# Kernel optimization log

Hardware: AMD Instinct MI355X
Metric: run time of the kernel (lower is better)

Reference implementation:

```python
import jax, jax.numpy as jnp
import numpy as np

HEADS, KV_HEADS, HEAD_DIM = 16, 4, 128
WINDOW, ROPE_THETA, EPS = 512, 10000.0, 1e-6


def _rms_norm(x, w):
    # Gemma RMSNorm: float32 compute, scale = 1 + w
    xf = x.astype(jnp.float32)
    y = xf * jax.lax.rsqrt(jnp.mean(xf * xf, axis=-1, keepdims=True) + EPS)
    return (y * (1.0 + w.astype(jnp.float32))).astype(x.dtype)


def _rope_cos_sin(T, dtype):
    inv_freq = 1.0 / ROPE_THETA ** (jnp.arange(0, HEAD_DIM, 2, dtype=jnp.float32) / HEAD_DIM)
    pos = jnp.arange(T, dtype=jnp.float32)
    freqs = pos[:, None] * inv_freq[None, :]          # [T, Dh/2]
    emb = jnp.concatenate([freqs, freqs], axis=-1)    # [T, Dh]
    return emb.astype(dtype), emb  # cos/sin applied below


def _rotate_half(x):
    x1, x2 = jnp.split(x, 2, axis=-1)
    return jnp.concatenate([-x2, x1], axis=-1)


def setup_inputs() -> dict:
    key = jax.random.key(0)
    ks = jax.random.split(key, 7)
    B, T, D = 2, 2048, 2048
    s = lambda k, shape, fan: jax.random.normal(k, shape, jnp.float32) * (fan ** -0.5)
    return {
        "x": jax.random.normal(ks[0], (B, T, D), jnp.float32),
        "Wq": s(ks[1], (HEADS * HEAD_DIM, D), D),
        "Wk": s(ks[2], (KV_HEADS * HEAD_DIM, D), D),
        "Wv": s(ks[3], (KV_HEADS * HEAD_DIM, D), D),
        "Wo": s(ks[4], (D, HEADS * HEAD_DIM), HEADS * HEAD_DIM),
        "qn_w": jax.random.normal(ks[5], (HEAD_DIM,), jnp.float32) * 0.02,
        "kn_w": jax.random.normal(ks[6], (HEAD_DIM,), jnp.float32) * 0.02,
    }


def reference(x, Wq, Wk, Wv, Wo, qn_w, kn_w):
    B, T, D = x.shape
    H, Hkv, Dh = HEADS, KV_HEADS, HEAD_DIM
    G = H // Hkv

    q = (x @ Wq.T).reshape(B, T, H, Dh).transpose(0, 2, 1, 3)     # [B,H,T,Dh]
    k = (x @ Wk.T).reshape(B, T, Hkv, Dh).transpose(0, 2, 1, 3)   # [B,Hkv,T,Dh]
    v = (x @ Wv.T).reshape(B, T, Hkv, Dh).transpose(0, 2, 1, 3)

    q = _rms_norm(q, qn_w)
    k = _rms_norm(k, kn_w)

    emb_c, emb_f = _rope_cos_sin(T, x.dtype)
    cos = jnp.cos(emb_f).astype(x.dtype)[None, None]  # [1,1,T,Dh]
    sin = jnp.sin(emb_f).astype(x.dtype)[None, None]
    q = q * cos + _rotate_half(q) * sin
    k = k * cos + _rotate_half(k) * sin

    q = q * (Dh ** -0.5)
    qg = q.reshape(B, Hkv, G, T, Dh)

    scores = jnp.einsum('bhgtd,bhkd->bhgtk', qg.astype(jnp.float32), k.astype(jnp.float32))

    dist = jnp.arange(T)[:, None] - jnp.arange(T)[None, :]        # [T,T]
    mask = (dist >= 0) & (dist <= WINDOW)
    scores = jnp.where(mask[None, None, None], scores, jnp.finfo(jnp.float32).min)
    att = jax.nn.softmax(scores, axis=-1).astype(x.dtype)

    ctx = jnp.einsum('bhgtk,bhkd->bhgtd', att, v)                 # [B,Hkv,G,T,Dh]
    out = ctx.reshape(B, H, T, Dh).transpose(0, 2, 1, 3).reshape(B, T, H * Dh)
    return out @ Wo.T
```

## Files before the change

### kernel.cpp

```cpp
#include <hip/hip_runtime.h>
#include <stdint.h>


typedef __attribute__((ext_vector_type(8))) short bf16x8;
typedef __attribute__((ext_vector_type(4))) float f32x4;

typedef __attribute__((address_space(3))) unsigned int lds_u32;
typedef const __attribute__((address_space(1))) unsigned int glb_u32;

#define LOG2E 1.44269504088896340736f

__device__ __forceinline__ unsigned short f2bf(float f) {
  unsigned int x = __builtin_bit_cast(unsigned int, f);
  x += 0x7FFFu + ((x >> 16) & 1u);
  return (unsigned short)(x >> 16);
}

__global__ __launch_bounds__(256) void castall(const float* __restrict__ x,
                                               const float* __restrict__ wq,
                                               const float* __restrict__ wk,
                                               const float* __restrict__ wv,
                                               const float* __restrict__ wo,
                                               unsigned short* __restrict__ xb,
                                               unsigned short* __restrict__ wqkvb,
                                               unsigned short* __restrict__ wob) {
  int i = blockIdx.x * 256 + threadIdx.x;
  const float* src;
  unsigned short* dst;
  int off;
  if (i < 2097152)       { src = x;  dst = xb;              off = i; }
  else if (i < 3145728)  { src = wq; dst = wqkvb;           off = i - 2097152; }
  else if (i < 3407872)  { src = wk; dst = wqkvb + 4194304; off = i - 3145728; }
  else if (i < 3670016)  { src = wv; dst = wqkvb + 5242880; off = i - 3407872; }
  else                   { src = wo; dst = wob;             off = i - 3670016; }
  float4 v = ((const float4*)src)[off];
  uint2 o;
  o.x = (unsigned)f2bf(v.x) | ((unsigned)f2bf(v.y) << 16);
  o.y = (unsigned)f2bf(v.z) | ((unsigned)f2bf(v.w) << 16);
  ((uint2*)dst)[off] = o;
}

__global__ __launch_bounds__(256) void rope_tab(float* __restrict__ c,
                                                float* __restrict__ s) {
  int idx = blockIdx.x * 256 + threadIdx.x;
  int t = idx >> 6, i = idx & 63;
  float invf = exp2f(-(float)i * (13.287712379549449f / 64.0f));
  float a = (float)t * invf;
  c[idx] = cosf(a);
  s[idx] = sinf(a);
}

template <int BN>
__global__ __launch_bounds__(512, 2) void gemm256(const unsigned short* __restrict__ A,
                                                  const unsigned short* __restrict__ Bm,
                                                  float* __restrict__ C,
                                                  int N, int K) {
  constexpr int BSL = BN * 128;
  __shared__ uint8_t lds[65536 + 2 * BSL];
  const int tid = threadIdx.x, lane = tid & 63, w = tid >> 6;
  const int wm = w >> 2, wn = w & 3;
  const size_t m0 = (size_t)blockIdx.y * 256, n0 = (size_t)blockIdx.x * BN;
  const int srow = lane >> 3;
  const int schunk = (lane & 7) ^ srow;

  f32x4 acc[8][BN / 64];
#pragma unroll
  for (int i = 0; i < 8; ++i)
#pragma unroll
    for (int j = 0; j < BN / 64; ++j) acc[i][j] = f32x4{0.f, 0.f, 0.f, 0.f};

  const int NT = K >> 6;

  auto stageA = [&](int t, int par) {
    uint8_t* slot = lds + (par << 15);
#pragma unroll
    for (int j = 0; j < 4; ++j) {
      int r0 = (j * 8 + w) * 8;
      const unsigned short* src =
          A + (m0 + r0 + srow) * (size_t)K + t * 64 + schunk * 8;
      __builtin_amdgcn_global_load_lds((glb_u32*)src,
                                       (lds_u32*)(slot + r0 * 128), 16, 0, 0);
    }
  };
  auto stageB = [&](int t, int par) {
    uint8_t* slot = lds + 65536 + par * BSL;
#pragma unroll
    for (int j = 0; j < BN / 64; ++j) {
      int r0 = (j * 8 + w) * 8;
      const unsigned short* src =
          Bm + (n0 + r0 + srow) * (size_t)K + t * 64 + schunk * 8;
      __builtin_amdgcn_global_load_lds((glb_u32*)src,
                                       (lds_u32*)(slot + r0 * 128), 16, 0, 0);
    }
  };
  auto compute = [&](int par, int h) {
    const uint8_t* Asl = lds + (par << 15);
    const uint8_t* Bsl = lds + 65536 + par * BSL;
    bf16x8 af[8], bf[BN / 64];
    const int x7 = lane & 7;
    const int cx = h * 4 + (lane >> 4);
    const int rab = wm * 128 + (lane & 15);
    const int rbb = wn * (BN / 4) + (lane & 15);
#pragma unroll
    for (int mt = 0; mt < 8; ++mt)
      af[mt] = *(const bf16x8*)(Asl + (rab + mt * 16) * 128 + ((cx ^ x7) << 4));
#pragma unroll
    for (int nt = 0; nt < BN / 64; ++nt)
      bf[nt] = *(const bf16x8*)(Bsl + (rbb + nt * 16) * 128 + ((cx ^ x7) << 4));
    __builtin_amdgcn_s_setprio(1);
#pragma unroll
    for (int mt = 0; mt < 8; ++mt)
#pragma unroll
      for (int nt = 0; nt < BN / 64; ++nt)
        acc[mt][nt] = __builtin_amdgcn_mfma_f32_16x16x32_bf16(
            af[mt], bf[nt], acc[mt][nt], 0, 0, 0);
    __builtin_amdgcn_s_setprio(0);
  };

  stageA(0, 0);
  stageB(0, 0);
  for (int t = 0; t < NT - 1; ++t) {
    const int p = t & 1, q = p ^ 1;
    stageA(t + 1, q);
    asm volatile("s_waitcnt vmcnt(4)" ::: "memory");
    __builtin_amdgcn_s_barrier();
    __builtin_amdgcn_sched_barrier(0);
    compute(p, 0);
    stageB(t + 1, q);
    compute(p, 1);
    asm volatile("" ::: "memory");
    __builtin_amdgcn_s_barrier();
    __builtin_amdgcn_sched_barrier(0);
  }
  {
    const int p = (NT - 1) & 1;
    asm volatile("s_waitcnt vmcnt(0)" ::: "memory");
    __builtin_amdgcn_s_barrier();
    __builtin_amdgcn_sched_barrier(0);
    compute(p, 0);
    compute(p, 1);
  }
#pragma unroll
  for (int mt = 0; mt < 8; ++mt)
#pragma unroll
    for (int nt = 0; nt < BN / 64; ++nt) {
      size_t row = m0 + wm * 128 + mt * 16 + (lane >> 4) * 4;
      size_t col = n0 + wn * (BN / 4) + nt * 16 + (lane & 15);
#pragma unroll
      for (int r = 0; r < 4; ++r)
        C[(row + r) * N + col] = acc[mt][nt][r];
    }
}

__global__ __launch_bounds__(256) void eplg(const float* __restrict__ qkv,
                                            const float* __restrict__ qw,
                                            const float* __restrict__ kw,
                                            const float* __restrict__ rc,
                                            const float* __restrict__ rs,
                                            unsigned short* __restrict__ qb,
                                            unsigned short* __restrict__ kb) {
  const int row = blockIdx.x;
  const int t = row & 2047;
  const int lane = threadIdx.x & 63, w = threadIdx.x >> 6;
  const float* base = qkv + (size_t)row * 3072;
  const int d0 = 2 * lane;
  const float c0 = rc[t * 64 + (d0 & 63)];
  const float c1 = rc[t * 64 + ((d0 + 1) & 63)];
  const float s0 = rs[t * 64 + (d0 & 63)];
  const float s1 = rs[t * 64 + ((d0 + 1) & 63)];
  const float sgn = (lane < 32) ? -1.0f : 1.0f;

#pragma unroll
  for (int hh = 0; hh < 4; ++hh) {
    int h = w * 4 + hh;
    float2 x = *(const float2*)(base + h * 128 + d0);
    float ss = x.x * x.x + x.y * x.y;
#pragma unroll
    for (int m = 1; m < 64; m <<= 1) ss += __shfl_xor(ss, m);
    float r = rsqrtf(ss * (1.0f / 128.0f) + 1e-6f);
    float y0 = x.x * r * (1.0f + qw[d0]);
    float y1 = x.y * r * (1.0f + qw[d0 + 1]);
    float p0 = __shfl_xor(y0, 32);
    float p1 = __shfl_xor(y1, 32);
    float o0 = (y0 * c0 + sgn * p0 * s0) * 0.08838834764831845f;
    float o1 = (y1 * c1 + sgn * p1 * s1) * 0.08838834764831845f;
    unsigned int pk = (unsigned)f2bf(o0) | ((unsigned)f2bf(o1) << 16);
    *(unsigned int*)(qb + (size_t)row * 2048 + h * 128 + d0) = pk;
  }
  {
    float2 x = *(const float2*)(base + 2048 + w * 128 + d0);
    float ss = x.x * x.x + x.y * x.y;
#pragma unroll
    for (int m = 1; m < 64; m <<= 1) ss += __shfl_xor(ss, m);
    float r = rsqrtf(ss * (1.0f / 128.0f) + 1e-6f);
    float y0 = x.x * r * (1.0f + kw[d0]);
    float y1 = x.y * r * (1.0f + kw[d0 + 1]);
    float p0 = __shfl_xor(y0, 32);
    float p1 = __shfl_xor(y1, 32);
    float o0 = y0 * c0 + sgn * p0 * s0;
    float o1 = y1 * c1 + sgn * p1 * s1;
    unsigned int pk = (unsigned)f2bf(o0) | ((unsigned)f2bf(o1) << 16);
    *(unsigned int*)(kb + (size_t)row * 512 + w * 128 + d0) = pk;
  }
}

__global__ __launch_bounds__(256) void vtrans(const float* __restrict__ qkvf,
                                              unsigned short* __restrict__ vbt) {
  __shared__ float tile[64][65];
  const int t0 = blockIdx.x * 64;
  const int d0 = blockIdx.y * 64;
  const int b = blockIdx.z;
  const int tid = threadIdx.x;
#pragma unroll
  for (int i = 0; i < 4; ++i) {
    int idx = tid + 256 * i;
    int r = idx >> 4, c4 = idx & 15;
    float4 v = *(const float4*)(qkvf + (size_t)(b * 2048 + t0 + r) * 3072 +
                                2560 + d0 + c4 * 4);
    tile[r][c4 * 4 + 0] = v.x;
    tile[r][c4 * 4 + 1] = v.y;
    tile[r][c4 * 4 + 2] = v.z;
    tile[r][c4 * 4 + 3] = v.w;
  }
  __syncthreads();
  const int dr = tid >> 2, ts = (tid & 3) * 16;
  unsigned short tmp[16];
#pragma unroll
  for (int j = 0; j < 16; ++j) tmp[j] = f2bf(tile[ts + j][dr]);
  uint4* dst = (uint4*)(vbt + (size_t)(b * 512 + d0 + dr) * 2048 + t0 + ts);
  dst[0] = *(uint4*)(tmp);
  dst[1] = *(uint4*)(tmp + 8);
}

__global__ __launch_bounds__(256) void attn(const unsigned short* __restrict__ qb,
                                            const unsigned short* __restrict__ kb,
                                            const unsigned short* __restrict__ vbt,
                                            unsigned short* __restrict__ ctxb) {
  __shared__ uint8_t Ks[64 * 256];
  __shared__ uint8_t Vs[128 * 128];
  __shared__ uint8_t Ps[4][16 * 128];
  const int qi = blockIdx.x, h = blockIdx.y, b = blockIdx.z;
  const int kvh = h >> 2;
  const int t0 = qi * 64;
  const int tid = threadIdx.x, lane = tid & 63, w = tid >> 6;

  bf16x8 qf[4];
  {
    int qrow = t0 + w * 16 + (lane & 15);
    const unsigned short* qp =
        qb + (size_t)(b * 2048 + qrow) * 2048 + h * 128 + (lane >> 4) * 8;
#pragma unroll
    for (int kc = 0; kc < 4; ++kc) qf[kc] = *(const bf16x8*)(qp + kc * 32);
  }
  f32x4 of[8];
#pragma unroll
  for (int i = 0; i < 8; ++i) of[i] = f32x4{0.f, 0.f, 0.f, 0.f};
  float m_run[4], l_run[4];
#pragma unroll
  for (int r = 0; r < 4; ++r) { m_run[r] = -1e30f; l_run[r] = 0.0f; }

  int kt0 = t0 - 512; if (kt0 < 0) kt0 = 0;
  const int nt = (t0 + 64 - kt0) >> 6;
  uint8_t* Pw = Ps[w];

  for (int it = 0; it < nt; ++it) {
    const int kt = kt0 + (it << 6);
    __syncthreads();
#pragma unroll
    for (int i = 0; i < 4; ++i) {
      int c = tid + 256 * i;
      int krow = c >> 4, kcin = c & 15;
      uint4 kv = *(const uint4*)(kb + (size_t)(b * 2048 + kt + krow) * 512 +
                                 kvh * 128 + kcin * 8);
      *(uint4*)(Ks + krow * 256 + ((kcin * 16) ^ ((krow & 7) << 4))) = kv;
      int vrow = c >> 3, vcin = c & 7;
      uint4 vv = *(const uint4*)(vbt + (size_t)(b * 512 + kvh * 128 + vrow) * 2048 +
                                 kt + vcin * 8);
      *(uint4*)(Vs + vrow * 128 + ((vcin * 16) ^ ((vrow & 7) << 4))) = vv;
    }
    __syncthreads();

    f32x4 sf[4];
#pragma unroll
    for (int nc = 0; nc < 4; ++nc) {
      f32x4 s = f32x4{0.f, 0.f, 0.f, 0.f};
      int key = nc * 16 + (lane & 15);
#pragma unroll
      for (int kc = 0; kc < 4; ++kc) {
        bf16x8 kf = *(const bf16x8*)(
            Ks + key * 256 + (((lane >> 4) * 16 + kc * 64) ^ ((key & 7) << 4)));
        s = __builtin_amdgcn_mfma_f32_16x16x32_bf16(qf[kc], kf, s, 0, 0, 0);
      }
      sf[nc] = s;
    }
#pragma unroll
    for (int nc = 0; nc < 4; ++nc) {
      int j = kt + nc * 16 + (lane & 15);
#pragma unroll
      for (int r = 0; r < 4; ++r) {
        int tq = t0 + w * 16 + (lane >> 4) * 4 + r;
        if (!((j <= tq) && (tq - j <= 512))) sf[nc][r] = -1e30f;
      }
    }
    float alpha[4];
#pragma unroll
    for (int r = 0; r < 4; ++r) {
      float mx = fmaxf(fmaxf(sf[0][r], sf[1][r]), fmaxf(sf[2][r], sf[3][r]));
      mx = fmaxf(mx, __shfl_xor(mx, 1));
      mx = fmaxf(mx, __shfl_xor(mx, 2));
      mx = fmaxf(mx, __shfl_xor(mx, 4));
      mx = fmaxf(mx, __shfl_xor(mx, 8));
      float mn = fmaxf(m_run[r], mx);
      alpha[r] = exp2f((m_run[r] - mn) * LOG2E);
      m_run[r] = mn;
    }
    float l_add[4] = {0.f, 0.f, 0.f, 0.f};
#pragma unroll
    for (int nc = 0; nc < 4; ++nc)
#pragma unroll
      for (int r = 0; r < 4; ++r) {
        float p = exp2f((sf[nc][r] - m_run[r]) * LOG2E);
        sf[nc][r] = p;
        l_add[r] += p;
      }
#pragma unroll
    for (int r = 0; r < 4; ++r) {
      float la = l_add[r];
      la += __shfl_xor(la, 1);
      la += __shfl_xor(la, 2);
      la += __shfl_xor(la, 4);
      la += __shfl_xor(la, 8);
      l_run[r] = l_run[r] * alpha[r] + la;
    }
#pragma unroll
    for (int i = 0; i < 8; ++i)
#pragma unroll
      for (int r = 0; r < 4; ++r) of[i][r] *= alpha[r];

#pragma unroll
    for (int nc = 0; nc < 4; ++nc) {
      int key = nc * 16 + (lane & 15);
#pragma unroll
      for (int r = 0; r < 4; ++r) {
        int prow = (lane >> 4) * 4 + r;
        *(unsigned short*)(Pw + prow * 128 + ((key * 2) ^ ((prow & 7) << 4))) =
            f2bf(sf[nc][r]);
      }
    }
#pragma unroll
    for (int ks = 0; ks < 2; ++ks) {
      int prow = lane & 15;
      bf16x8 pf = *(const bf16x8*)(
          Pw + prow * 128 + ((ks * 64 + (lane >> 4) * 16) ^ ((prow & 7) << 4)));
#pragma unroll
      for (int nc8 = 0; nc8 < 8; ++nc8) {
        int vrow = nc8 * 16 + (lane & 15);
        bf16x8 vf = *(const bf16x8*)(
            Vs + vrow * 128 + ((ks * 64 + (lane >> 4) * 16) ^ ((vrow & 7) << 4)));
        of[nc8] = __builtin_amdgcn_mfma_f32_16x16x32_bf16(pf, vf, of[nc8], 0, 0, 0);
      }
    }
  }
#pragma unroll
  for (int nc8 = 0; nc8 < 8; ++nc8)
#pragma unroll
    for (int r = 0; r < 4; ++r) {
      int tq = t0 + w * 16 + (lane >> 4) * 4 + r;
      int col = h * 128 + nc8 * 16 + (lane & 15);
      ctxb[(size_t)(b * 2048 + tq) * 2048 + col] = f2bf(of[nc8][r] / l_run[r]);
    }
}

extern "C" void kernel_launch(void* const* d_in, const int* in_sizes, int n_in,
                              void* d_out, int out_size, void* d_ws, size_t ws_size,
                              hipStream_t stream) {
  const float* x  = (const float*)d_in[0];
  const float* Wq = (const float*)d_in[1];
  const float* Wk = (const float*)d_in[2];
  const float* Wv = (const float*)d_in[3];
  const float* Wo = (const float*)d_in[4];
  const float* qw = (const float*)d_in[5];
  const float* kw = (const float*)d_in[6];

  uint8_t* ws = (uint8_t*)d_ws;
  if (ws_size < 131072000ull) return;
  unsigned short* xb    = (unsigned short*)(ws);
  unsigned short* wqkvb = (unsigned short*)(ws + 16777216);
  unsigned short* wob   = (unsigned short*)(ws + 29360128);
  float*          qkvf  = (float*)(ws + 37748736);
  unsigned short* qb2   = (unsigned short*)(ws + 88080384);
  unsigned short* kb2   = (unsigned short*)(ws + 104857600);
  unsigned short* vbt   = (unsigned short*)(ws + 109051904);
  unsigned short* ctxb  = (unsigned short*)(ws + 113246208);
  float*          ropec = (float*)(ws + 130023424);
  float*          ropes = (float*)(ws + 130547712);

  castall<<<18432, 256, 0, stream>>>(x, Wq, Wk, Wv, Wo, xb, wqkvb, wob);
  rope_tab<<<512, 256, 0, stream>>>(ropec, ropes);
  {
    dim3 g(3072 / 256, 4096 / 256);
    gemm256<256><<<g, 512, 0, stream>>>(xb, wqkvb, qkvf, 3072, 2048);
  }
  eplg<<<4096, 256, 0, stream>>>(qkvf, qw, kw, ropec, ropes, qb2, kb2);
  {
    dim3 g(32, 8, 2);
    vtrans<<<g, 256, 0, stream>>>(qkvf, vbt);
  }
  {
    dim3 g(32, 16, 2);
    attn<<<g, 256, 0, stream>>>(qb2, kb2, vbt, ctxb);
  }
  {
    dim3 g(2048 / 128, 4096 / 256);
    gemm256<128><<<g, 512, 0, stream>>>(ctxb, wob, (float*)d_out, 2048, 2048);
  }
}
```

Baseline: 294.5 us.

## Share K/V tiles across GQA heads with double-buffered async LDS loads and lazy rescale

```diff
diff --git a/kernel.cpp b/kernel.cpp
--- a/kernel.cpp
+++ b/kernel.cpp
@@ -7,8 +7,6 @@
 
 typedef __attribute__((address_space(3))) unsigned int lds_u32;
 typedef const __attribute__((address_space(1))) unsigned int glb_u32;
-
-#define LOG2E 1.44269504088896340736f
 
 __device__ __forceinline__ unsigned short f2bf(float f) {
   unsigned int x = __builtin_bit_cast(unsigned int, f);
@@ -169,6 +167,7 @@
   const float s0 = rs[t * 64 + (d0 & 63)];
   const float s1 = rs[t * 64 + ((d0 + 1) & 63)];
   const float sgn = (lane < 32) ? -1.0f : 1.0f;
+  const float QS = 0.12751744817f;
 
 #pragma unroll
   for (int hh = 0; hh < 4; ++hh) {
@@ -182,8 +181,8 @@
     float y1 = x.y * r * (1.0f + qw[d0 + 1]);
     float p0 = __shfl_xor(y0, 32);
     float p1 = __shfl_xor(y1, 32);
-    float o0 = (y0 * c0 + sgn * p0 * s0) * 0.08838834764831845f;
-    float o1 = (y1 * c1 + sgn * p1 * s1) * 0.08838834764831845f;
+    float o0 = (y0 * c0 + sgn * p0 * s0) * QS;
+    float o1 = (y1 * c1 + sgn * p1 * s1) * QS;
     unsigned int pk = (unsigned)f2bf(o0) | ((unsigned)f2bf(o1) << 16);
     *(unsigned int*)(qb + (size_t)row * 2048 + h * 128 + d0) = pk;
   }
@@ -232,21 +231,21 @@
   dst[1] = *(uint4*)(tmp + 8);
 }
 
-__global__ __launch_bounds__(256) void attn(const unsigned short* __restrict__ qb,
-                                            const unsigned short* __restrict__ kb,
-                                            const unsigned short* __restrict__ vbt,
-                                            unsigned short* __restrict__ ctxb) {
-  __shared__ uint8_t Ks[64 * 256];
-  __shared__ uint8_t Vs[128 * 128];
-  __shared__ uint8_t Ps[4][16 * 128];
-  const int qi = blockIdx.x, h = blockIdx.y, b = blockIdx.z;
-  const int kvh = h >> 2;
+__global__ __launch_bounds__(1024) void attn(const unsigned short* __restrict__ qb,
+                                             const unsigned short* __restrict__ kb,
+                                             const unsigned short* __restrict__ vbt,
+                                             unsigned short* __restrict__ ctxb) {
+  __shared__ uint8_t Ks[2][64 * 256];
+  __shared__ uint8_t Vs[2][128 * 128];
+  __shared__ uint8_t Ps[16][16 * 128];
+  const int qi = blockIdx.x, kvh = blockIdx.y, b = blockIdx.z;
   const int t0 = qi * 64;
   const int tid = threadIdx.x, lane = tid & 63, w = tid >> 6;
+  const int h = kvh * 4 + (w & 3), wq = w >> 2;
 
   bf16x8 qf[4];
   {
-    int qrow = t0 + w * 16 + (lane & 15);
+    int qrow = t0 + wq * 16 + (lane & 15);
     const unsigned short* qp =
         qb + (size_t)(b * 2048 + qrow) * 2048 + h * 128 + (lane >> 4) * 8;
 #pragma unroll
@@ -263,22 +262,34 @@
   const int nt = (t0 + 64 - kt0) >> 6;
   uint8_t* Pw = Ps[w];
 
+  const int krow_s = 4 * w + (lane >> 4);
+  const int kchunk_s = (lane & 15) ^ (krow_s & 7);
+  const int vrow_s = 8 * w + (lane >> 3);
+  const int vchunk_s = (lane & 7) ^ (vrow_s & 7);
+  auto stage = [&](int it, int par) {
+    int kt = kt0 + (it << 6);
+    const unsigned short* ksrc =
+        kb + (size_t)(b * 2048 + kt + krow_s) * 512 + kvh * 128 + kchunk_s * 8;
+    __builtin_amdgcn_global_load_lds((glb_u32*)ksrc,
+                                     (lds_u32*)(&Ks[par][w * 1024]), 16, 0, 0);
+    const unsigned short* vsrc =
+        vbt + (size_t)(b * 512 + kvh * 128 + vrow_s) * 2048 + kt + vchunk_s * 8;
+    __builtin_amdgcn_global_load_lds((glb_u32*)vsrc,
+                                     (lds_u32*)(&Vs[par][w * 1024]), 16, 0, 0);
+  };
+
+  stage(0, 0);
   for (int it = 0; it < nt; ++it) {
+    const int par = it & 1;
     const int kt = kt0 + (it << 6);
-    __syncthreads();
-#pragma unroll
-    for (int i = 0; i < 4; ++i) {
-      int c = tid + 256 * i;
-      int krow = c >> 4, kcin = c & 15;
-      uint4 kv = *(const uint4*)(kb + (size_t)(b * 2048 + kt + krow) * 512 +
-                                 kvh * 128 + kcin * 8);
-      *(uint4*)(Ks + krow * 256 + ((kcin * 16) ^ ((krow & 7) << 4))) = kv;
-      int vrow = c >> 3, vcin = c & 7;
-      uint4 vv = *(const uint4*)(vbt + (size_t)(b * 512 + kvh * 128 + vrow) * 2048 +
-                                 kt + vcin * 8);
-      *(uint4*)(Vs + vrow * 128 + ((vcin * 16) ^ ((vrow & 7) << 4))) = vv;
-    }
-    __syncthreads();
+    if (it + 1 < nt) {
+      stage(it + 1, par ^ 1);
+      asm volatile("s_waitcnt vmcnt(2)" ::: "memory");
+    } else {
+      asm volatile("s_waitcnt vmcnt(0)" ::: "memory");
+    }
+    __builtin_amdgcn_s_barrier();
+    __builtin_amdgcn_sched_barrier(0);
 
     f32x4 sf[4];
 #pragma unroll
@@ -288,7 +299,7 @@
 #pragma unroll
       for (int kc = 0; kc < 4; ++kc) {
         bf16x8 kf = *(const bf16x8*)(
-            Ks + key * 256 + (((lane >> 4) * 16 + kc * 64) ^ ((key & 7) << 4)));
+            Ks[par] + key * 256 + (((lane >> 4) * 16 + kc * 64) ^ ((key & 7) << 4)));
         s = __builtin_amdgcn_mfma_f32_16x16x32_bf16(qf[kc], kf, s, 0, 0, 0);
       }
       sf[nc] = s;
@@ -298,28 +309,42 @@
       int j = kt + nc * 16 + (lane & 15);
 #pragma unroll
       for (int r = 0; r < 4; ++r) {
-        int tq = t0 + w * 16 + (lane >> 4) * 4 + r;
+        int tq = t0 + wq * 16 + (lane >> 4) * 4 + r;
         if (!((j <= tq) && (tq - j <= 512))) sf[nc][r] = -1e30f;
       }
     }
-    float alpha[4];
+    float mx[4];
 #pragma unroll
     for (int r = 0; r < 4; ++r) {
-      float mx = fmaxf(fmaxf(sf[0][r], sf[1][r]), fmaxf(sf[2][r], sf[3][r]));
-      mx = fmaxf(mx, __shfl_xor(mx, 1));
-      mx = fmaxf(mx, __shfl_xor(mx, 2));
-      mx = fmaxf(mx, __shfl_xor(mx, 4));
-      mx = fmaxf(mx, __shfl_xor(mx, 8));
-      float mn = fmaxf(m_run[r], mx);
-      alpha[r] = exp2f((m_run[r] - mn) * LOG2E);
-      m_run[r] = mn;
+      float m = fmaxf(fmaxf(sf[0][r], sf[1][r]), fmaxf(sf[2][r], sf[3][r]));
+      m = fmaxf(m, __shfl_xor(m, 1));
+      m = fmaxf(m, __shfl_xor(m, 2));
+      m = fmaxf(m, __shfl_xor(m, 4));
+      m = fmaxf(m, __shfl_xor(m, 8));
+      mx[r] = m;
+    }
+    bool grow = (mx[0] > m_run[0] + 8.0f) | (mx[1] > m_run[1] + 8.0f) |
+                (mx[2] > m_run[2] + 8.0f) | (mx[3] > m_run[3] + 8.0f);
+    if (__any(grow)) {
+      float alpha[4];
+#pragma unroll
+      for (int r = 0; r < 4; ++r) {
+        float mn = fmaxf(m_run[r], mx[r]);
+        alpha[r] = exp2f(m_run[r] - mn);
+        m_run[r] = mn;
+        l_run[r] *= alpha[r];
+      }
+#pragma unroll
+      for (int i = 0; i < 8; ++i)
+#pragma unroll
+        for (int r = 0; r < 4; ++r) of[i][r] *= alpha[r];
     }
     float l_add[4] = {0.f, 0.f, 0.f, 0.f};
 #pragma unroll
     for (int nc = 0; nc < 4; ++nc)
 #pragma unroll
       for (int r = 0; r < 4; ++r) {
-        float p = exp2f((sf[nc][r] - m_run[r]) * LOG2E);
+        float p = exp2f(sf[nc][r] - m_run[r]);
         sf[nc][r] = p;
         l_add[r] += p;
       }
@@ -330,13 +355,8 @@
       la += __shfl_xor(la, 2);
       la += __shfl_xor(la, 4);
       la += __shfl_xor(la, 8);
-      l_run[r] = l_run[r] * alpha[r] + la;
-    }
-#pragma unroll
-    for (int i = 0; i < 8; ++i)
-#pragma unroll
-      for (int r = 0; r < 4; ++r) of[i][r] *= alpha[r];
-
+      l_run[r] += la;
+    }
 #pragma unroll
     for (int nc = 0; nc < 4; ++nc) {
       int key = nc * 16 + (lane & 15);
@@ -356,16 +376,19 @@
       for (int nc8 = 0; nc8 < 8; ++nc8) {
         int vrow = nc8 * 16 + (lane & 15);
         bf16x8 vf = *(const bf16x8*)(
-            Vs + vrow * 128 + ((ks * 64 + (lane >> 4) * 16) ^ ((vrow & 7) << 4)));
+            Vs[par] + vrow * 128 + ((ks * 64 + (lane >> 4) * 16) ^ ((vrow & 7) << 4)));
         of[nc8] = __builtin_amdgcn_mfma_f32_16x16x32_bf16(pf, vf, of[nc8], 0, 0, 0);
       }
     }
+    asm volatile("" ::: "memory");
+    __builtin_amdgcn_s_barrier();
+    __builtin_amdgcn_sched_barrier(0);
   }
 #pragma unroll
   for (int nc8 = 0; nc8 < 8; ++nc8)
 #pragma unroll
     for (int r = 0; r < 4; ++r) {
-      int tq = t0 + w * 16 + (lane >> 4) * 4 + r;
+      int tq = t0 + wq * 16 + (lane >> 4) * 4 + r;
       int col = h * 128 + nc8 * 16 + (lane & 15);
       ctxb[(size_t)(b * 2048 + tq) * 2048 + col] = f2bf(of[nc8][r] / l_run[r]);
     }
@@ -407,8 +430,8 @@
     vtrans<<<g, 256, 0, stream>>>(qkvf, vbt);
   }
   {
-    dim3 g(32, 16, 2);
-    attn<<<g, 256, 0, stream>>>(qb2, kb2, vbt, ctxb);
+    dim3 g(32, 4, 2);
+    attn<<<g, 1024, 0, stream>>>(qb2, kb2, vbt, ctxb);
   }
   {
     dim3 g(2048 / 128, 4096 / 256);
```

Result: faster. 285.6 us (-3.0%).
